# Performance work log

Hardware: AMD Instinct MI355X
Metric: run time of the kernel (lower is better)

Reference implementation:

```python
import jax, jax.numpy as jnp
import numpy as np

B, H, S, D = 65536, 1024, 1024, 128  # batch, hidden_dim, memory_slots, slot_size
WRITE_THRESHOLD = 0.01


def setup_inputs() -> dict:
    key = jax.random.key(0)
    ks = jax.random.split(key, 6)
    return {
        "query": jax.random.normal(ks[0], (B, H), jnp.float32),
        "content": jax.random.normal(ks[1], (B, H), jnp.float32),
        "memory": jax.random.normal(ks[2], (S, D), jnp.float32),
        "memory_age": jnp.zeros((S,), jnp.float32),
        "W_read": jax.random.normal(ks[3], (H, S), jnp.float32) * 0.02,
        "b_read": jnp.zeros((S,), jnp.float32),
        "W_write": jax.random.normal(ks[4], (H, S), jnp.float32) * 0.02,
        "b_write": jnp.zeros((S,), jnp.float32),
        "W_content": jax.random.normal(ks[5], (H, D), jnp.float32) * 0.02,
        "b_content": jnp.zeros((D,), jnp.float32),
    }


def reference(query, content, memory, memory_age, W_read, b_read,
              W_write, b_write, W_content, b_content):
    # ---- read: attention-based addressing over memory slots ----
    read_weights = jax.nn.softmax(query @ W_read + b_read, axis=-1)   # [B, S]
    read_content = read_weights @ memory                              # [B, D]

    # ---- write: vectorized consolidation update (replaces per-slot python loop) ----
    write_weights = jax.nn.softmax(query @ W_write + b_write, axis=-1)  # [B, S]
    w_mean = write_weights.mean(axis=0)                                 # [S]
    c_mean = (content @ W_content + b_content).mean(axis=0)             # [D]
    mask = w_mean > WRITE_THRESHOLD                                     # [S] bool
    consolidation = jax.nn.sigmoid(memory_age * 0.1)                    # [S]
    f = (w_mean * consolidation)[:, None]                               # [S, 1]
    updated = (1.0 - f) * memory + f * c_mean[None, :]                  # [S, D]
    new_memory = jnp.where(mask[:, None], updated, memory)
    new_memory_age = memory_age + mask.astype(memory_age.dtype)

    return read_content, new_memory, new_memory_age
```

## Files before the change

kernel.cpp:

```cpp
#include <hip/hip_runtime.h>
#include <hip/hip_fp16.h>
#include <cstdint>
#include <cstddef>

#define B_N 65536
#define H_N 1024
#define S_N 1024
#define D_N 128

typedef __attribute__((ext_vector_type(8))) short bf16x8;
typedef __attribute__((ext_vector_type(8))) _Float16 f16x8;
typedef __attribute__((ext_vector_type(4))) float f32x4;

#define MFMA_BF(a, b, c) __builtin_amdgcn_mfma_f32_16x16x32_bf16((a), (b), (c), 0, 0, 0)
#define MFMA_F16(a, b, c) __builtin_amdgcn_mfma_f32_16x16x32_f16((a), (b), (c), 0, 0, 0)

__device__ __forceinline__ unsigned short f2bf(float f) {
    unsigned u = __float_as_uint(f);
    u += 0x7FFFu + ((u >> 16) & 1u);
    return (unsigned short)(u >> 16);
}
__device__ __forceinline__ float h2f(unsigned short h) {
    return __half2float(__ushort_as_half(h));
}
__device__ __forceinline__ unsigned short f2h(float f) {
    return __half_as_ushort(__float2half_rn(f));
}
__device__ __forceinline__ void async16(void* lds, const void* g) {
    __builtin_amdgcn_global_load_lds(
        (const __attribute__((address_space(1))) unsigned int*)g,
        (__attribute__((address_space(3))) unsigned int*)lds, 16, 0, 0);
}

__global__ void k_zero(float* p, int n) {
    int i = blockIdx.x * blockDim.x + threadIdx.x;
    if (i < n) p[i] = 0.f;
}

__global__ __launch_bounds__(256) void k_prep_q(const float* __restrict__ q,
                                                unsigned short* __restrict__ qb) {
    size_t i = ((size_t)blockIdx.x * 256 + threadIdx.x) * 8;
    float4 a = *(const float4*)(q + i);
    float4 b = *(const float4*)(q + i + 4);
    uint4 o;
    o.x = (unsigned)f2bf(a.x) | ((unsigned)f2bf(a.y) << 16);
    o.y = (unsigned)f2bf(a.z) | ((unsigned)f2bf(a.w) << 16);
    o.z = (unsigned)f2bf(b.x) | ((unsigned)f2bf(b.y) << 16);
    o.w = (unsigned)f2bf(b.z) | ((unsigned)f2bf(b.w) << 16);
    *(uint4*)(qb + i) = o;
}

__global__ __launch_bounds__(256) void k_prep_w(const float* __restrict__ Wr,
                                                const float* __restrict__ Ww,
                                                unsigned short* __restrict__ wcat) {
    __shared__ float t[32][33];
    const int kb = blockIdx.x * 32, nb = blockIdx.y * 32;
    const float* src = blockIdx.z ? Ww : Wr;
    const int tx = threadIdx.x & 31, ty = threadIdx.x >> 5;
#pragma unroll
    for (int i = 0; i < 4; i++) {
        int r = ty + i * 8;
        t[r][tx] = src[(size_t)(kb + r) * S_N + nb + tx];
    }
    __syncthreads();
    unsigned short* dst = wcat + (size_t)blockIdx.z * 1024 * 1024;
#pragma unroll
    for (int i = 0; i < 4; i++) {
        int r = ty + i * 8;
        dst[(size_t)(nb + r) * 1024 + kb + tx] = f2bf(t[tx][r]);
    }
}

__global__ __launch_bounds__(256) void k_prep_mem(const float* __restrict__ mem,
                                                  unsigned short* __restrict__ memT) {
    __shared__ float t[32][33];
    const int db = blockIdx.x * 32, sb = blockIdx.y * 32;
    const int tx = threadIdx.x & 31, ty = threadIdx.x >> 5;
#pragma unroll
    for (int i = 0; i < 4; i++) {
        int r = ty + i * 8;
        t[r][tx] = mem[(size_t)(sb + r) * D_N + db + tx];
    }
    __syncthreads();
#pragma unroll
    for (int i = 0; i < 4; i++) {
        int r = ty + i * 8;
        memT[(size_t)(db + r) * 1024 + sb + tx] = f2h(t[tx][r]);
    }
}

__global__ __launch_bounds__(256) void k_content(const float* __restrict__ content,
                                                 float* __restrict__ csum) {
    const int tid = threadIdx.x;
    const size_t r0 = (size_t)blockIdx.x * 128;
    float4 a = {0.f, 0.f, 0.f, 0.f};
    const float* base = content + r0 * H_N + tid * 4;
#pragma unroll 8
    for (int r = 0; r < 128; r++) {
        float4 v = *(const float4*)(base + (size_t)r * H_N);
        a.x += v.x; a.y += v.y; a.z += v.z; a.w += v.w;
    }
    atomicAdd(&csum[tid * 4 + 0], a.x);
    atomicAdd(&csum[tid * 4 + 1], a.y);
    atomicAdd(&csum[tid * 4 + 2], a.z);
    atomicAdd(&csum[tid * 4 + 3], a.w);
}

__global__ __launch_bounds__(256) void k_gemm(const unsigned short* __restrict__ qb,
                                              const unsigned short* __restrict__ wcat,
                                              const float* __restrict__ b_read,
                                              const float* __restrict__ b_write,
                                              unsigned short* __restrict__ logits) {
    __shared__ unsigned short aL[4096];
    __shared__ unsigned short bL[4096];
    const int tid = threadIdx.x;
    const int wave = tid >> 6, lane = tid & 63;
    const int wm = wave >> 1, wn = wave & 1;
    const int l16 = lane & 15, g = lane >> 4;
    const int nb = blockIdx.x;
    const size_t mrow = (size_t)blockIdx.y * 128;

    f32x4 acc[4][4];
#pragma unroll
    for (int i = 0; i < 4; i++)
#pragma unroll
        for (int j = 0; j < 4; j++) acc[i][j] = (f32x4){0.f, 0.f, 0.f, 0.f};

    const int a0 = tid >> 2;
    const int s0 = ((tid & 3) ^ ((a0 >> 1) & 3)) * 8;
    const unsigned short* wbase = wcat + (size_t)nb * 128 * 1024;
    const unsigned short* srcA = qb + (mrow + a0) * 1024 + s0;
    const unsigned short* srcB = wbase + (size_t)a0 * 1024 + s0;

    for (int k0 = 0; k0 < 1024; k0 += 32) {
        __syncthreads();
        async16((char*)aL + wave * 1024, srcA + k0);
        async16((char*)aL + 4096 + wave * 1024, srcA + 64 * 1024 + k0);
        async16((char*)bL + wave * 1024, srcB + k0);
        async16((char*)bL + 4096 + wave * 1024, srcB + 64 * 1024 + k0);
        __syncthreads();

        bf16x8 af[4], bv[4];
#pragma unroll
        for (int mt = 0; mt < 4; mt++) {
            int m = wm * 64 + mt * 16 + l16;
            int phys = m * 4 + (g ^ ((m >> 1) & 3));
            af[mt] = *(const bf16x8*)&aL[phys * 8];
        }
#pragma unroll
        for (int nt = 0; nt < 4; nt++) {
            int n = wn * 64 + nt * 16 + l16;
            int phys = n * 4 + (g ^ ((n >> 1) & 3));
            bv[nt] = *(const bf16x8*)&bL[phys * 8];
        }
#pragma unroll
        for (int mt = 0; mt < 4; mt++)
#pragma unroll
            for (int nt = 0; nt < 4; nt++)
                acc[mt][nt] = MFMA_BF(af[mt], bv[nt], acc[mt][nt]);
    }

    const float* bias = (nb < 8) ? b_read : b_write;
    const int cadj = (nb < 8) ? nb * 128 : nb * 128 - 1024;
#pragma unroll
    for (int nt = 0; nt < 4; nt++) {
        const int col = wn * 64 + nt * 16 + l16;
        const float bvv = bias[cadj + col];
#pragma unroll
        for (int mt = 0; mt < 4; mt++) {
            const int row = wm * 64 + mt * 16 + g * 4;
#pragma unroll
            for (int r = 0; r < 4; r++) {
                float e = __expf(acc[mt][nt][r] + bvv);
                logits[(mrow + row + r) * 2048 + nb * 128 + col] = f2h(e);
            }
        }
    }
}

__global__ __launch_bounds__(256) void k_post(const unsigned short* __restrict__ logits,
                                              const unsigned short* __restrict__ memT,
                                              float* __restrict__ out,
                                              float* __restrict__ wpart, int blk0) {
    __shared__ unsigned short L[16 * 2056];
    __shared__ float sInvR[16], sInvW[16];
    const int tid = threadIdx.x;
    const size_t r0 = (size_t)blockIdx.x * 16;
#pragma unroll
    for (int i = 0; i < 16; i++) {
        int c2 = i * 256 + tid;
        int r = c2 >> 8, off = (c2 & 255) * 8;
        *(uint4*)&L[r * 2056 + off] = *(const uint4*)&logits[(r0 + r) * 2048 + off];
    }
    __syncthreads();
    {
        const int r = tid >> 4, sub = tid & 15;
        const unsigned* row = (const unsigned*)&L[r * 2056];
        float zr = 0.f, zw = 0.f;
#pragma unroll 8
        for (int i = 0; i < 32; i++) {
            unsigned u = row[i * 16 + sub];
            zr += h2f((unsigned short)(u & 0xffff)) + h2f((unsigned short)(u >> 16));
            unsigned v = row[512 + i * 16 + sub];
            zw += h2f((unsigned short)(v & 0xffff)) + h2f((unsigned short)(v >> 16));
        }
        zr += __shfl_xor(zr, 1); zr += __shfl_xor(zr, 2);
        zr += __shfl_xor(zr, 4); zr += __shfl_xor(zr, 8);
        zw += __shfl_xor(zw, 1); zw += __shfl_xor(zw, 2);
        zw += __shfl_xor(zw, 4); zw += __shfl_xor(zw, 8);
        if (sub == 0) { sInvR[r] = 1.f / zr; sInvW[r] = 1.f / zw; }
    }
    __syncthreads();
    const int wave = tid >> 6, lane = tid & 63;
    const int l16 = lane & 15, g = lane >> 4;
    f32x4 acc0 = (f32x4){0.f, 0.f, 0.f, 0.f}, acc1 = acc0;
    for (int k0 = 0; k0 < 1024; k0 += 32) {
        f16x8 a  = *(const f16x8*)&L[l16 * 2056 + k0 + g * 8];
        f16x8 b0 = *(const f16x8*)&memT[(size_t)(wave * 32 + l16) * 1024 + k0 + g * 8];
        f16x8 b1 = *(const f16x8*)&memT[(size_t)(wave * 32 + 16 + l16) * 1024 + k0 + g * 8];
        acc0 = MFMA_F16(a, b0, acc0);
        acc1 = MFMA_F16(a, b1, acc1);
    }
#pragma unroll
    for (int r = 0; r < 4; r++) {
        int row = g * 4 + r;
        float iz = sInvR[row];
        out[(r0 + row) * D_N + wave * 32 + l16] = acc0[r] * iz;
        out[(r0 + row) * D_N + wave * 32 + 16 + l16] = acc1[r] * iz;
    }
    float c0 = 0.f, c1 = 0.f, c2 = 0.f, c3 = 0.f;
#pragma unroll
    for (int r = 0; r < 16; r++) {
        float iz = sInvW[r];
        uint2 u = *(const uint2*)&L[r * 2056 + 1024 + tid * 4];
        c0 += h2f((unsigned short)(u.x & 0xffff)) * iz;
        c1 += h2f((unsigned short)(u.x >> 16)) * iz;
        c2 += h2f((unsigned short)(u.y & 0xffff)) * iz;
        c3 += h2f((unsigned short)(u.y >> 16)) * iz;
    }
    float4 o = {c0, c1, c2, c3};
    *(float4*)&wpart[(size_t)(blk0 + blockIdx.x) * 1024 + tid * 4] = o;
}

__global__ __launch_bounds__(256) void k_wreduce(const float* __restrict__ wpart,
                                                 float* __restrict__ wsum) {
    const int c = (blockIdx.x & 3) * 256 + threadIdx.x;
    const int i0 = (blockIdx.x >> 2) * 512;
    float s0 = 0.f, s1 = 0.f;
    for (int i = 0; i < 512; i += 2) {
        s0 += wpart[(size_t)(i0 + i) * 1024 + c];
        s1 += wpart[(size_t)(i0 + i + 1) * 1024 + c];
    }
    atomicAdd(&wsum[c], s0 + s1);
}

__global__ void k_cmean(const float* __restrict__ csum, const float* __restrict__ Wc,
                        const float* __restrict__ bc, float* __restrict__ cmean) {
    const int d = blockIdx.x, t = threadIdx.x;
    float s = 0.f;
#pragma unroll
    for (int j = 0; j < 16; j++) {
        int h = j * 64 + t;
        s += csum[h] * Wc[h * D_N + d];
    }
#pragma unroll
    for (int o = 1; o < 64; o <<= 1) s += __shfl_xor(s, o);
    if (t == 0) cmean[d] = s * (1.0f / (float)B_N) + bc[d];
}

__global__ __launch_bounds__(256) void k_final(const float* __restrict__ memory,
                                               const float* __restrict__ age,
                                               const float* __restrict__ wsum,
                                               const float* __restrict__ cmean,
                                               float* __restrict__ out) {
    const int idx = blockIdx.x * 256 + threadIdx.x;
    const int s = idx >> 7, d = idx & 127;
    const float wm = wsum[s] * (1.0f / (float)B_N);
    const bool mask = wm > 0.01f;
    const float cons = 1.0f / (1.0f + __expf(-0.1f * age[s]));
    const float f = wm * cons;
    const float m = memory[idx];
    const float nm = mask ? ((1.0f - f) * m + f * cmean[d]) : m;
    out[(size_t)B_N * D_N + idx] = nm;
    if (d == 0) out[(size_t)B_N * D_N + (size_t)S_N * D_N + s] = age[s] + (mask ? 1.0f : 0.0f);
}

extern "C" void kernel_launch(void* const* d_in, const int* in_sizes, int n_in,
                              void* d_out, int out_size, void* d_ws, size_t ws_size,
                              hipStream_t stream) {
    const float* query    = (const float*)d_in[0];
    const float* content  = (const float*)d_in[1];
    const float* memory   = (const float*)d_in[2];
    const float* age      = (const float*)d_in[3];
    const float* W_read   = (const float*)d_in[4];
    const float* b_read   = (const float*)d_in[5];
    const float* W_write  = (const float*)d_in[6];
    const float* b_write  = (const float*)d_in[7];
    const float* W_cont   = (const float*)d_in[8];
    const float* b_cont   = (const float*)d_in[9];

    char* ws = (char*)d_ws;
    unsigned short* wcat   = (unsigned short*)ws;
    unsigned short* memT   = (unsigned short*)(ws + (4u << 20));
    float* csum            = (float*)(ws + 4456448);
    float* wsum            = csum + 1024;
    float* cmean           = csum + 2048;
    float* wpart           = (float*)(ws + (8u << 20));
    char* dynbase          = ws + (24u << 20);
    float* out = (float*)d_out;

    long long avail = (long long)ws_size - (24ll << 20);
    long long maxrows = avail > 0 ? avail / 6144 : 0;
    int CB = (int)((maxrows / 128) * 128);
    if (CB > B_N) CB = B_N;
    if (CB < 128) CB = 128;
    unsigned short* qbf    = (unsigned short*)dynbase;
    unsigned short* logits = (unsigned short*)(dynbase + (size_t)CB * 2048);

    k_zero<<<8, 256, 0, stream>>>(csum, 2048);
    k_prep_w<<<dim3(32, 32, 2), 256, 0, stream>>>(W_read, W_write, wcat);
    k_prep_mem<<<dim3(4, 32), 256, 0, stream>>>(memory, memT);
    k_content<<<512, 256, 0, stream>>>(content, csum);

    for (int s0 = 0; s0 < B_N; s0 += CB) {
        int rows = B_N - s0;
        if (rows > CB) rows = CB;
        k_prep_q<<<rows / 2, 256, 0, stream>>>(query + (size_t)s0 * H_N, qbf);
        k_gemm<<<dim3(16, rows / 128), 256, 0, stream>>>(qbf, wcat, b_read, b_write, logits);
        k_post<<<rows / 16, 256, 0, stream>>>(logits, memT, out + (size_t)s0 * D_N,
                                              wpart, s0 / 16);
    }
    k_wreduce<<<32, 256, 0, stream>>>(wpart, wsum);
    k_cmean<<<128, 64, 0, stream>>>(csum, W_cont, b_cont, cmean);
    k_final<<<512, 256, 0, stream>>>(memory, age, wsum, cmean, out);
}
```

Measured before the change: 1.164 ms.

## Fuse softmax row sums into GEMM epilogue and split post kernel

The GEMM epilogue now accumulates per-row exp sums and writes partial row sums per column block, so the post kernel no longer rescans logits to compute normalizers. The old monolithic k_post is split into a row-normalizer kernel, a read GEMM kernel with 64-row blocks reading logits directly from global, and a write column-sum kernel over 256-row slabs. The GEMM grid is also remapped so 8 consecutive blocks share a column block of weights for L2 locality. The trade-off is extra kernel launches and re-reading logits from global twice instead of once via LDS.

```diff
diff --git a/kernel.cpp b/kernel.cpp
--- a/kernel.cpp
+++ b/kernel.cpp
@@ -110,15 +110,20 @@
                                               const unsigned short* __restrict__ wcat,
                                               const float* __restrict__ b_read,
                                               const float* __restrict__ b_write,
-                                              unsigned short* __restrict__ logits) {
+                                              unsigned short* __restrict__ logits,
+                                              float* __restrict__ wrp, int rowoff) {
     __shared__ unsigned short aL[4096];
     __shared__ unsigned short bL[4096];
+    __shared__ float zb[2][128];
     const int tid = threadIdx.x;
     const int wave = tid >> 6, lane = tid & 63;
     const int wm = wave >> 1, wn = wave & 1;
     const int l16 = lane & 15, g = lane >> 4;
-    const int nb = blockIdx.x;
-    const size_t mrow = (size_t)blockIdx.y * 128;
+    const int F = blockIdx.x;
+    const int x8 = F & 7, q = F >> 3;
+    const int nb = q & 15;
+    const int mb = x8 + 8 * (q >> 4);
+    const size_t mrow = (size_t)mb * 128;
 
     f32x4 acc[4][4];
 #pragma unroll
@@ -162,6 +167,11 @@
 
     const float* bias = (nb < 8) ? b_read : b_write;
     const int cadj = (nb < 8) ? nb * 128 : nb * 128 - 1024;
+    float rs[4][4];
+#pragma unroll
+    for (int i = 0; i < 4; i++)
+#pragma unroll
+        for (int j = 0; j < 4; j++) rs[i][j] = 0.f;
 #pragma unroll
     for (int nt = 0; nt < 4; nt++) {
         const int col = wn * 64 + nt * 16 + l16;
@@ -172,86 +182,98 @@
 #pragma unroll
             for (int r = 0; r < 4; r++) {
                 float e = __expf(acc[mt][nt][r] + bvv);
+                rs[mt][r] += e;
                 logits[(mrow + row + r) * 2048 + nb * 128 + col] = f2h(e);
             }
         }
     }
-}
-
-__global__ __launch_bounds__(256) void k_post(const unsigned short* __restrict__ logits,
+#pragma unroll
+    for (int mt = 0; mt < 4; mt++)
+#pragma unroll
+        for (int r = 0; r < 4; r++) {
+            float v = rs[mt][r];
+            v += __shfl_xor(v, 1); v += __shfl_xor(v, 2);
+            v += __shfl_xor(v, 4); v += __shfl_xor(v, 8);
+            rs[mt][r] = v;
+        }
+    if (l16 == 0) {
+#pragma unroll
+        for (int mt = 0; mt < 4; mt++)
+#pragma unroll
+            for (int r = 0; r < 4; r++)
+                zb[wn][wm * 64 + mt * 16 + g * 4 + r] = rs[mt][r];
+    }
+    __syncthreads();
+    if (tid < 128)
+        wrp[(size_t)nb * B_N + rowoff + mrow + tid] = zb[0][tid] + zb[1][tid];
+}
+
+__global__ __launch_bounds__(256) void k_rowz(const float* __restrict__ wrp,
+                                              float* __restrict__ zinv, int rowoff) {
+    const int row = rowoff + blockIdx.x * 256 + threadIdx.x;
+    float sr = 0.f, sw = 0.f;
+#pragma unroll
+    for (int nb = 0; nb < 8; nb++) sr += wrp[(size_t)nb * B_N + row];
+#pragma unroll
+    for (int nb = 8; nb < 16; nb++) sw += wrp[(size_t)nb * B_N + row];
+    zinv[row] = 1.f / sr;
+    zinv[B_N + row] = 1.f / sw;
+}
+
+__global__ __launch_bounds__(256) void k_read(const unsigned short* __restrict__ logits,
                                               const unsigned short* __restrict__ memT,
-                                              float* __restrict__ out,
-                                              float* __restrict__ wpart, int blk0) {
-    __shared__ unsigned short L[16 * 2056];
-    __shared__ float sInvR[16], sInvW[16];
+                                              const float* __restrict__ zr,
+                                              float* __restrict__ out) {
+    const int wave = threadIdx.x >> 6, lane = threadIdx.x & 63;
+    const int l16 = lane & 15, g = lane >> 4;
+    const int r0 = blockIdx.x * 64 + wave * 16;
+    f32x4 acc[8];
+#pragma unroll
+    for (int i = 0; i < 8; i++) acc[i] = (f32x4){0.f, 0.f, 0.f, 0.f};
+    const unsigned short* arow = logits + (size_t)(r0 + l16) * 2048;
+    for (int k0 = 0; k0 < 1024; k0 += 32) {
+        f16x8 a = *(const f16x8*)&arow[k0 + g * 8];
+#pragma unroll
+        for (int nt = 0; nt < 8; nt++) {
+            f16x8 b = *(const f16x8*)&memT[(size_t)(nt * 16 + l16) * 1024 + k0 + g * 8];
+            acc[nt] = MFMA_F16(a, b, acc[nt]);
+        }
+    }
+#pragma unroll
+    for (int rr = 0; rr < 4; rr++) {
+        const int row = r0 + g * 4 + rr;
+        const float iz = zr[row];
+#pragma unroll
+        for (int nt = 0; nt < 8; nt++)
+            out[(size_t)row * D_N + nt * 16 + l16] = acc[nt][rr] * iz;
+    }
+}
+
+__global__ __launch_bounds__(256) void k_wcol(const unsigned short* __restrict__ logits,
+                                              const float* __restrict__ zw,
+                                              float* __restrict__ wpart, int slab0) {
     const int tid = threadIdx.x;
-    const size_t r0 = (size_t)blockIdx.x * 16;
-#pragma unroll
-    for (int i = 0; i < 16; i++) {
-        int c2 = i * 256 + tid;
-        int r = c2 >> 8, off = (c2 & 255) * 8;
-        *(uint4*)&L[r * 2056 + off] = *(const uint4*)&logits[(r0 + r) * 2048 + off];
-    }
-    __syncthreads();
-    {
-        const int r = tid >> 4, sub = tid & 15;
-        const unsigned* row = (const unsigned*)&L[r * 2056];
-        float zr = 0.f, zw = 0.f;
-#pragma unroll 8
-        for (int i = 0; i < 32; i++) {
-            unsigned u = row[i * 16 + sub];
-            zr += h2f((unsigned short)(u & 0xffff)) + h2f((unsigned short)(u >> 16));
-            unsigned v = row[512 + i * 16 + sub];
-            zw += h2f((unsigned short)(v & 0xffff)) + h2f((unsigned short)(v >> 16));
-        }
-        zr += __shfl_xor(zr, 1); zr += __shfl_xor(zr, 2);
-        zr += __shfl_xor(zr, 4); zr += __shfl_xor(zr, 8);
-        zw += __shfl_xor(zw, 1); zw += __shfl_xor(zw, 2);
-        zw += __shfl_xor(zw, 4); zw += __shfl_xor(zw, 8);
-        if (sub == 0) { sInvR[r] = 1.f / zr; sInvW[r] = 1.f / zw; }
-    }
-    __syncthreads();
-    const int wave = tid >> 6, lane = tid & 63;
-    const int l16 = lane & 15, g = lane >> 4;
-    f32x4 acc0 = (f32x4){0.f, 0.f, 0.f, 0.f}, acc1 = acc0;
-    for (int k0 = 0; k0 < 1024; k0 += 32) {
-        f16x8 a  = *(const f16x8*)&L[l16 * 2056 + k0 + g * 8];
-        f16x8 b0 = *(const f16x8*)&memT[(size_t)(wave * 32 + l16) * 1024 + k0 + g * 8];
-        f16x8 b1 = *(const f16x8*)&memT[(size_t)(wave * 32 + 16 + l16) * 1024 + k0 + g * 8];
-        acc0 = MFMA_F16(a, b0, acc0);
-        acc1 = MFMA_F16(a, b1, acc1);
-    }
-#pragma unroll
-    for (int r = 0; r < 4; r++) {
-        int row = g * 4 + r;
-        float iz = sInvR[row];
-        out[(r0 + row) * D_N + wave * 32 + l16] = acc0[r] * iz;
-        out[(r0 + row) * D_N + wave * 32 + 16 + l16] = acc1[r] * iz;
-    }
+    const int r0 = blockIdx.x * 256;
     float c0 = 0.f, c1 = 0.f, c2 = 0.f, c3 = 0.f;
-#pragma unroll
-    for (int r = 0; r < 16; r++) {
-        float iz = sInvW[r];
-        uint2 u = *(const uint2*)&L[r * 2056 + 1024 + tid * 4];
+#pragma unroll 4
+    for (int r = 0; r < 256; r++) {
+        const float iz = zw[r0 + r];
+        uint2 u = *(const uint2*)&logits[(size_t)(r0 + r) * 2048 + 1024 + tid * 4];
         c0 += h2f((unsigned short)(u.x & 0xffff)) * iz;
         c1 += h2f((unsigned short)(u.x >> 16)) * iz;
         c2 += h2f((unsigned short)(u.y & 0xffff)) * iz;
         c3 += h2f((unsigned short)(u.y >> 16)) * iz;
     }
     float4 o = {c0, c1, c2, c3};
-    *(float4*)&wpart[(size_t)(blk0 + blockIdx.x) * 1024 + tid * 4] = o;
+    *(float4*)&wpart[(size_t)(slab0 + blockIdx.x) * 1024 + tid * 4] = o;
 }
 
 __global__ __launch_bounds__(256) void k_wreduce(const float* __restrict__ wpart,
                                                  float* __restrict__ wsum) {
-    const int c = (blockIdx.x & 3) * 256 + threadIdx.x;
-    const int i0 = (blockIdx.x >> 2) * 512;
-    float s0 = 0.f, s1 = 0.f;
-    for (int i = 0; i < 512; i += 2) {
-        s0 += wpart[(size_t)(i0 + i) * 1024 + c];
-        s1 += wpart[(size_t)(i0 + i + 1) * 1024 + c];
-    }
-    atomicAdd(&wsum[c], s0 + s1);
+    const int c = blockIdx.x * 256 + threadIdx.x;
+    float s = 0.f;
+    for (int i = 0; i < 256; i++) s += wpart[(size_t)i * 1024 + c];
+    wsum[c] = s;
 }
 
 __global__ void k_cmean(const float* __restrict__ csum, const float* __restrict__ Wc,
@@ -300,24 +322,26 @@
     const float* b_cont   = (const float*)d_in[9];
 
     char* ws = (char*)d_ws;
-    unsigned short* wcat   = (unsigned short*)ws;
-    unsigned short* memT   = (unsigned short*)(ws + (4u << 20));
-    float* csum            = (float*)(ws + 4456448);
-    float* wsum            = csum + 1024;
-    float* cmean           = csum + 2048;
-    float* wpart           = (float*)(ws + (8u << 20));
-    char* dynbase          = ws + (24u << 20);
+    unsigned short* wcat = (unsigned short*)ws;
+    unsigned short* memT = (unsigned short*)(ws + (4u << 20));
+    float* csum  = (float*)(ws + (4u << 20) + (256u << 10));
+    float* wsum  = csum + 1024;
+    float* cmean = csum + 2048;
+    float* wrp   = (float*)(ws + (5u << 20));
+    float* zinv  = (float*)(ws + (9u << 20));
+    float* wpart = (float*)(ws + (9u << 20) + (512u << 10));
+    char* dynbase = ws + (11u << 20);
     float* out = (float*)d_out;
 
-    long long avail = (long long)ws_size - (24ll << 20);
+    long long avail = (long long)ws_size - (11ll << 20);
     long long maxrows = avail > 0 ? avail / 6144 : 0;
-    int CB = (int)((maxrows / 128) * 128);
+    int CB = (int)((maxrows / 1024) * 1024);
     if (CB > B_N) CB = B_N;
-    if (CB < 128) CB = 128;
+    if (CB < 1024) CB = 1024;
     unsigned short* qbf    = (unsigned short*)dynbase;
     unsigned short* logits = (unsigned short*)(dynbase + (size_t)CB * 2048);
 
-    k_zero<<<8, 256, 0, stream>>>(csum, 2048);
+    k_zero<<<4, 256, 0, stream>>>(csum, 1024);
     k_prep_w<<<dim3(32, 32, 2), 256, 0, stream>>>(W_read, W_write, wcat);
     k_prep_mem<<<dim3(4, 32), 256, 0, stream>>>(memory, memT);
     k_content<<<512, 256, 0, stream>>>(content, csum);
@@ -326,11 +350,14 @@
         int rows = B_N - s0;
         if (rows > CB) rows = CB;
         k_prep_q<<<rows / 2, 256, 0, stream>>>(query + (size_t)s0 * H_N, qbf);
-        k_gemm<<<dim3(16, rows / 128), 256, 0, stream>>>(qbf, wcat, b_read, b_write, logits);
-        k_post<<<rows / 16, 256, 0, stream>>>(logits, memT, out + (size_t)s0 * D_N,
-                                              wpart, s0 / 16);
-    }
-    k_wreduce<<<32, 256, 0, stream>>>(wpart, wsum);
+        k_gemm<<<(rows / 128) * 16, 256, 0, stream>>>(qbf, wcat, b_read, b_write,
+                                                      logits, wrp, s0);
+        k_rowz<<<rows / 256, 256, 0, stream>>>(wrp, zinv, s0);
+        k_read<<<rows / 64, 256, 0, stream>>>(logits, memT, zinv + s0,
+                                              out + (size_t)s0 * D_N);
+        k_wcol<<<rows / 256, 256, 0, stream>>>(logits, zinv + B_N + s0, wpart, s0 / 256);
+    }
+    k_wreduce<<<4, 256, 0, stream>>>(wpart, wsum);
     k_cmean<<<128, 64, 0, stream>>>(csum, W_cont, b_cont, cmean);
     k_final<<<512, 256, 0, stream>>>(memory, age, wsum, cmean, out);
 }
```

New measurement: 1.268 ms. 1.09x slower.
